# Kernel optimization log

Hardware: AMD Instinct MI355X
Metric: run time of the kernel (lower is better)

The kernel has to match this reference:

```python
import jax, jax.numpy as jnp
import numpy as np

N_NODES = 50000
N_EDGES = 800000
NODE_DIM = 128
EDGE_IN = 31
EMB_DIM = 128
GATE_HID = 128
INIT_GATE_BIAS = 2.0


def setup_inputs() -> dict:
    key = jax.random.key(0)
    ks = jax.random.split(key, 8)
    x = jax.random.normal(ks[0], (N_NODES, NODE_DIM), dtype=jnp.float32)
    edge_attr = jax.random.normal(ks[1], (N_EDGES, EDGE_IN), dtype=jnp.float32)
    edge_index = jax.random.randint(ks[2], (2, N_EDGES), 0, N_NODES, dtype=jnp.int64)
    gate_in_dim = 2 * NODE_DIM + EDGE_IN
    # params (torch.nn.Linear-style scaled uniform init)
    def lin(k, fan_in, fan_out):
        bound = 1.0 / np.sqrt(fan_in)
        kw, kb = jax.random.split(k)
        W = jax.random.uniform(kw, (fan_in, fan_out), minval=-bound, maxval=bound, dtype=jnp.float32)
        b = jax.random.uniform(kb, (fan_out,), minval=-bound, maxval=bound, dtype=jnp.float32)
        return W, b
    W_proj, b_proj = lin(ks[3], EDGE_IN, EMB_DIM)
    W1, b1 = lin(ks[4], gate_in_dim, GATE_HID)
    W2, _ = lin(ks[5], GATE_HID, 1)
    b2 = jnp.full((1,), INIT_GATE_BIAS, dtype=jnp.float32)
    return {
        "x": x,
        "edge_attr": edge_attr,
        "edge_index": edge_index,
        "W_proj": W_proj,
        "b_proj": b_proj,
        "W1": W1,
        "b1": b1,
        "W2": W2,
        "b2": b2,
    }


def reference(x, edge_attr, edge_index, W_proj, b_proj, W1, b1, W2, b2):
    src = edge_index[0]
    dst = edge_index[1]
    xu = x[src]                      # [E, node_dim] gather
    xv = x[dst]                      # [E, node_dim] gather
    base = edge_attr @ W_proj + b_proj            # [E, emb_dim]
    gate_in = jnp.concatenate([xu, xv, edge_attr], axis=-1)  # [E, 2*node_dim+31]
    h = jax.nn.gelu(gate_in @ W1 + b1)            # [E, gate_hidden]
    gate = jax.nn.sigmoid(h @ W2 + b2)            # [E, 1]
    return base * gate                            # [E, emb_dim]
```

## Files before the change

### kernel.cpp

```cpp
#include <hip/hip_runtime.h>
#include <math.h>

#define N_NODES 50000
#define N_EDGES 800000

typedef __attribute__((ext_vector_type(8))) short bf16x8;
typedef __attribute__((ext_vector_type(4))) float f32x4;

__device__ __forceinline__ unsigned f2bfu(float f) {
  union { float f; unsigned u; } v; v.f = f;
  return (v.u + 0x7FFFu + ((v.u >> 16) & 1u)) >> 16;
}
__device__ __forceinline__ short f2bf(float f) { return (short)f2bfu(f); }

__device__ __forceinline__ float bflo(unsigned d) {
  union { unsigned u; float f; } v; v.u = d << 16; return v.f;
}
__device__ __forceinline__ float bfhi(unsigned d) {
  union { unsigned u; float f; } v; v.u = d & 0xFFFF0000u; return v.f;
}

__device__ __forceinline__ float gelu_f(float h) {
  const float m1 = h * h;
  const float t2u = h * fmaf(0.07135481f, m1, 1.5957691f);
  const float e = __expf(t2u);
  const float rc = __builtin_amdgcn_rcpf(1.f + e);
  return h - h * rc;
}

#define PIN(v) asm volatile("" : "+v"(v))

__global__ void wfrag_kernel(const float* __restrict__ W_proj,
                             const float* __restrict__ W1,
                             uint4* __restrict__ wfrag) {
  const int id = threadIdx.x;
  const int mat = id >> 9;
  const int fid = id & 511;
  const int mb = fid >> 6, ln = fid & 63;
  const int rr = ln & 15, gg = ln >> 4;
  const float* W = mat ? W_proj : (W1 + (size_t)256 * 128);
  union { uint4 u; bf16x8 b; } f;
#pragma unroll
  for (int t = 0; t < 8; ++t) {
    const int kk = gg * 8 + t;
    f.b[t] = (kk < 31) ? f2bf(W[(size_t)kk * 128 + 16 * mb + rr]) : (short)0;
  }
  wfrag[id] = f.u;
}

__global__ __launch_bounds__(256) void node_kernel(
    const float* __restrict__ x, const float* __restrict__ W1,
    const float* __restrict__ b1, unsigned short* __restrict__ AB) {
  const int l = threadIdx.x & 63;
  const int wv = threadIdx.x >> 6;
  const int r = l & 15, g4 = l >> 4;

  const int wid = blockIdx.x * 4 + wv;
  const int s = wid & 3;

  bf16x8 wA[4][4];
#pragma unroll
  for (int q = 0; q < 4; ++q) {
    const int c = 16 * (4 * s + q) + r;
    const float* Wb = (c < 128) ? (W1 + c) : (W1 + 128 * 128 + (c - 128));
#pragma unroll
    for (int ks = 0; ks < 4; ++ks) {
#pragma unroll
      for (int t = 0; t < 8; ++t)
        wA[q][ks][t] = f2bf(Wb[(size_t)(ks * 32 + g4 * 8 + t) * 128]);
      PIN(wA[q][ks]);
    }
  }
  float4 bv[4];
#pragma unroll
  for (int q = 0; q < 4; ++q)
    bv[q] = *(const float4*)(b1 + ((16 * (4 * s + q) + g4 * 4) & 127));

  const int half = s >> 1;

  for (int t0 = wid >> 2; t0 < (N_NODES / 16); t0 += 1024) {
    const int n0 = t0 * 16;
    f32x4 acc[4] = {{0,0,0,0},{0,0,0,0},{0,0,0,0},{0,0,0,0}};
#pragma unroll
    for (int ks = 0; ks < 4; ++ks) {
      const float* xr = x + (size_t)(n0 + r) * 128 + ks * 32 + g4 * 8;
      const float4 x0 = *(const float4*)xr;
      const float4 x1 = *(const float4*)(xr + 4);
      bf16x8 xb;
      xb[0] = f2bf(x0.x); xb[1] = f2bf(x0.y); xb[2] = f2bf(x0.z); xb[3] = f2bf(x0.w);
      xb[4] = f2bf(x1.x); xb[5] = f2bf(x1.y); xb[6] = f2bf(x1.z); xb[7] = f2bf(x1.w);
#pragma unroll
      for (int q = 0; q < 4; ++q)
        acc[q] = __builtin_amdgcn_mfma_f32_16x16x32_bf16(wA[q][ks], xb, acc[q], 0, 0, 0);
    }
#pragma unroll
    for (int q = 0; q < 4; ++q) {
      const int mb8 = 4 * (s & 1) + q;
      const float o0 = acc[q][0] + 0.5f * bv[q].x;
      const float o1 = acc[q][1] + 0.5f * bv[q].y;
      const float o2 = acc[q][2] + 0.5f * bv[q].z;
      const float o3 = acc[q][3] + 0.5f * bv[q].w;
      uint2 pk;
      pk.x = f2bfu(o0) | (f2bfu(o1) << 16);
      pk.y = f2bfu(o2) | (f2bfu(o3) << 16);
      *(uint2*)(AB + (size_t)(n0 + r) * 256 + half * 128 + g4 * 32 + mb8 * 4) = pk;
    }
  }
}

__global__ __launch_bounds__(256) void edge_kernel(
    const float* __restrict__ edge_attr, const int* __restrict__ edge_index,
    const unsigned short* __restrict__ AB, const uint4* __restrict__ wfrag,
    const float* __restrict__ b_proj, const float* __restrict__ W2,
    const float* __restrict__ b2, float* __restrict__ out) {
  __shared__ float tlds[4][16 * 128];
  const int l = threadIdx.x & 63;
  const int wv = threadIdx.x >> 6;
  const int r = l & 15, g4 = l >> 4;
  float* const tl = &tlds[wv][0];

  bf16x8 wH[8];
#pragma unroll
  for (int mb = 0; mb < 8; ++mb) {
    union { uint4 u; bf16x8 b; } h;
    h.u = wfrag[mb * 64 + l];
    wH[mb] = h.b;
    PIN(wH[mb]);
  }
  const float b2v = b2[0];
  const uint4* wpp = wfrag + 512;

  const int nwaves = gridDim.x * 4;
  const int NT = N_EDGES / 16;

  int tile = blockIdx.x * 4 + wv;
  if (tile >= NT) return;
  int src = edge_index[tile * 16 + r];
  int dst = edge_index[N_EDGES + tile * 16 + r];

  for (; tile < NT; tile += nwaves) {
    const int e = tile * 16 + r;
    const int cs = src, cd = dst;

    const int tn = tile + nwaves;
    if (tn < NT) {
      src = edge_index[tn * 16 + r];
      dst = edge_index[N_EDGES + tn * 16 + r];
    }

    const float* ear = edge_attr + (size_t)e * 31 + g4 * 8;
    bf16x8 eb;
#pragma unroll
    for (int t = 0; t < 8; ++t) {
      const int kk = g4 * 8 + t;
      eb[t] = (kk < 31) ? f2bf(ear[t]) : (short)0;
    }

    const uint4* ap4 = (const uint4*)(AB + (size_t)cs * 256 + g4 * 32);
    const uint4* bp4 = (const uint4*)(AB + (size_t)cd * 256 + 128 + g4 * 32);
    uint4 ua[4], ub[4];
#pragma unroll
    for (int t = 0; t < 4; ++t) { ua[t] = ap4[t]; ub[t] = bp4[t]; }

    f32x4 acch[8];
#pragma unroll
    for (int t = 0; t < 4; ++t) {
      acch[2 * t][0]     = bflo(ua[t].x) + bflo(ub[t].x);
      acch[2 * t][1]     = bfhi(ua[t].x) + bfhi(ub[t].x);
      acch[2 * t][2]     = bflo(ua[t].y) + bflo(ub[t].y);
      acch[2 * t][3]     = bfhi(ua[t].y) + bfhi(ub[t].y);
      acch[2 * t + 1][0] = bflo(ua[t].z) + bflo(ub[t].z);
      acch[2 * t + 1][1] = bfhi(ua[t].z) + bfhi(ub[t].z);
      acch[2 * t + 1][2] = bflo(ua[t].w) + bflo(ub[t].w);
      acch[2 * t + 1][3] = bfhi(ua[t].w) + bfhi(ub[t].w);
    }
#pragma unroll
    for (int mb = 0; mb < 8; ++mb)
      acch[mb] = __builtin_amdgcn_mfma_f32_16x16x32_bf16(wH[mb], eb, acch[mb], 0, 0, 0);

    float lg = 0.f;
#pragma unroll
    for (int mb = 0; mb < 8; ++mb) {
      const float4 w2v = *(const float4*)(W2 + 16 * mb + g4 * 4);
      lg = fmaf(gelu_f(acch[mb][0]), w2v.x, lg);
      lg = fmaf(gelu_f(acch[mb][1]), w2v.y, lg);
      lg = fmaf(gelu_f(acch[mb][2]), w2v.z, lg);
      lg = fmaf(gelu_f(acch[mb][3]), w2v.w, lg);
    }
    lg += __shfl_xor(lg, 16);
    lg += __shfl_xor(lg, 32);
    const float gate = __builtin_amdgcn_rcpf(1.f + __expf(-(lg + b2v)));

    PIN(wpp);

#pragma unroll
    for (int mb = 0; mb < 8; ++mb) {
      union { uint4 u; bf16x8 b; } wp;
      wp.u = wpp[mb * 64 + l];
      f32x4 ac = __builtin_amdgcn_mfma_f32_16x16x32_bf16(
          wp.b, eb, (f32x4){0.f, 0.f, 0.f, 0.f}, 0, 0, 0);
      const float4 bp = *(const float4*)(b_proj + 16 * mb + 4 * g4);
      f32x4 o;
      o[0] = (ac[0] + bp.x) * gate;
      o[1] = (ac[1] + bp.y) * gate;
      o[2] = (ac[2] + bp.z) * gate;
      o[3] = (ac[3] + bp.w) * gate;
      const int col = 16 * mb + 4 * g4;
      *(f32x4*)(tl + 128 * r + (col ^ ((r & 7) << 2))) = o;
    }

    float* const obase = out + (size_t)tile * 16 * 128;
#pragma unroll
    for (int k = 0; k < 8; ++k) {
      const int row = 2 * k + (l >> 5);
      const int col = 4 * (l & 31);
      const f32x4 v = *(const f32x4*)(tl + 128 * row + (col ^ ((row & 7) << 2)));
      __builtin_nontemporal_store(v, (f32x4*)(obase + 256 * k + 4 * l));
    }
  }
}

extern "C" void kernel_launch(void* const* d_in, const int* in_sizes, int n_in,
                              void* d_out, int out_size, void* d_ws, size_t ws_size,
                              hipStream_t stream) {
  const float* x          = (const float*)d_in[0];
  const float* edge_attr  = (const float*)d_in[1];
  const int*   edge_index = (const int*)d_in[2];
  const float* W_proj     = (const float*)d_in[3];
  const float* b_proj     = (const float*)d_in[4];
  const float* W1         = (const float*)d_in[5];
  const float* b1         = (const float*)d_in[6];
  const float* W2         = (const float*)d_in[7];
  const float* b2         = (const float*)d_in[8];
  float* out = (float*)d_out;
  unsigned short* AB = (unsigned short*)d_ws;
  uint4* wfrag = (uint4*)(AB + (size_t)N_NODES * 256);

  hipLaunchKernelGGL(wfrag_kernel, dim3(1), dim3(1024), 0, stream,
                     W_proj, W1, wfrag);
  hipLaunchKernelGGL(node_kernel, dim3(1024), dim3(256), 0, stream,
                     x, W1, b1, AB);
  hipLaunchKernelGGL(edge_kernel, dim3(2048), dim3(256), 0, stream,
                     edge_attr, edge_index, AB, wfrag, b_proj, W2, b2,
                     out);
}
```

Before: 190.6 us.

## Software-pipeline edge gathers one tile ahead, fold b_proj into MFMA, stage W_proj in LDS

The edge kernel now prefetches the next tile's node-row gathers and edge attributes into registers while computing the current tile, with edge indices fetched two tiles ahead, so gather latency overlaps compute. The projection bias is folded into the W_proj fragment as a 32nd K-row multiplied by a constant 1.0 lane in the edge-attribute operand, removing the per-tile bias loads and adds. The W_proj fragments are staged once per block into shared memory instead of being reloaded from global memory each tile. This raises register pressure and LDS use, which may lower occupancy, and the bias is now rounded to bf16.

```diff
diff --git a/kernel.cpp b/kernel.cpp
--- a/kernel.cpp
+++ b/kernel.cpp
@@ -32,6 +32,7 @@
 
 __global__ void wfrag_kernel(const float* __restrict__ W_proj,
                              const float* __restrict__ W1,
+                             const float* __restrict__ b_proj,
                              uint4* __restrict__ wfrag) {
   const int id = threadIdx.x;
   const int mat = id >> 9;
@@ -43,7 +44,10 @@
 #pragma unroll
   for (int t = 0; t < 8; ++t) {
     const int kk = gg * 8 + t;
-    f.b[t] = (kk < 31) ? f2bf(W[(size_t)kk * 128 + 16 * mb + rr]) : (short)0;
+    float v = 0.f;
+    if (kk < 31) v = W[(size_t)kk * 128 + 16 * mb + rr];
+    else if (mat == 1 && kk == 31) v = b_proj[16 * mb + rr];
+    f.b[t] = f2bf(v);
   }
   wfrag[id] = f.u;
 }
@@ -111,13 +115,18 @@
 __global__ __launch_bounds__(256) void edge_kernel(
     const float* __restrict__ edge_attr, const int* __restrict__ edge_index,
     const unsigned short* __restrict__ AB, const uint4* __restrict__ wfrag,
-    const float* __restrict__ b_proj, const float* __restrict__ W2,
-    const float* __restrict__ b2, float* __restrict__ out) {
+    const float* __restrict__ W2, const float* __restrict__ b2,
+    float* __restrict__ out) {
   __shared__ float tlds[4][16 * 128];
-  const int l = threadIdx.x & 63;
-  const int wv = threadIdx.x >> 6;
+  __shared__ uint4 wPl[512];
+  const int tid = threadIdx.x;
+  const int l = tid & 63;
+  const int wv = tid >> 6;
   const int r = l & 15, g4 = l >> 4;
   float* const tl = &tlds[wv][0];
+
+  wPl[tid] = wfrag[512 + tid];
+  wPl[tid + 256] = wfrag[768 + tid];
 
   bf16x8 wH[8];
 #pragma unroll
@@ -128,39 +137,47 @@
     PIN(wH[mb]);
   }
   const float b2v = b2[0];
-  const uint4* wpp = wfrag + 512;
+  __syncthreads();
 
   const int nwaves = gridDim.x * 4;
   const int NT = N_EDGES / 16;
 
   int tile = blockIdx.x * 4 + wv;
   if (tile >= NT) return;
-  int src = edge_index[tile * 16 + r];
-  int dst = edge_index[N_EDGES + tile * 16 + r];
-
-  for (; tile < NT; tile += nwaves) {
+
+  int sA, dA;
+  uint4 ua[4], ub[4];
+  float ear[8];
+  {
     const int e = tile * 16 + r;
-    const int cs = src, cd = dst;
-
-    const int tn = tile + nwaves;
-    if (tn < NT) {
-      src = edge_index[tn * 16 + r];
-      dst = edge_index[N_EDGES + tn * 16 + r];
-    }
-
-    const float* ear = edge_attr + (size_t)e * 31 + g4 * 8;
-    bf16x8 eb;
-#pragma unroll
-    for (int t = 0; t < 8; ++t) {
-      const int kk = g4 * 8 + t;
-      eb[t] = (kk < 31) ? f2bf(ear[t]) : (short)0;
-    }
-
+    const int cs = edge_index[e];
+    const int cd = edge_index[N_EDGES + e];
     const uint4* ap4 = (const uint4*)(AB + (size_t)cs * 256 + g4 * 32);
     const uint4* bp4 = (const uint4*)(AB + (size_t)cd * 256 + 128 + g4 * 32);
-    uint4 ua[4], ub[4];
 #pragma unroll
     for (int t = 0; t < 4; ++t) { ua[t] = ap4[t]; ub[t] = bp4[t]; }
+    const float* earp = edge_attr + (size_t)e * 31 + g4 * 8;
+#pragma unroll
+    for (int t = 0; t < 8; ++t)
+      ear[t] = (g4 * 8 + t < 31) ? earp[t] : 0.f;
+    const int tn = tile + nwaves;
+    const int en = (tn < NT ? tn : tile) * 16 + r;
+    sA = edge_index[en];
+    dA = edge_index[N_EDGES + en];
+  }
+
+  for (; tile < NT; tile += nwaves) {
+    const int tn = tile + nwaves;
+    const int tn2 = tile + 2 * nwaves;
+
+    const int en2 = (tn2 < NT ? tn2 : tile) * 16 + r;
+    const int sB = edge_index[en2];
+    const int dB = edge_index[N_EDGES + en2];
+
+    bf16x8 eb;
+#pragma unroll
+    for (int t = 0; t < 8; ++t) eb[t] = f2bf(ear[t]);
+    if (g4 == 3) eb[7] = (short)0x3F80;
 
     f32x4 acch[8];
 #pragma unroll
@@ -174,6 +191,18 @@
       acch[2 * t + 1][2] = bflo(ua[t].w) + bflo(ub[t].w);
       acch[2 * t + 1][3] = bfhi(ua[t].w) + bfhi(ub[t].w);
     }
+
+    if (tn < NT) {
+      const uint4* ap4 = (const uint4*)(AB + (size_t)sA * 256 + g4 * 32);
+      const uint4* bp4 = (const uint4*)(AB + (size_t)dA * 256 + 128 + g4 * 32);
+#pragma unroll
+      for (int t = 0; t < 4; ++t) { ua[t] = ap4[t]; ub[t] = bp4[t]; }
+      const float* earp = edge_attr + (size_t)(tn * 16 + r) * 31 + g4 * 8;
+#pragma unroll
+      for (int t = 0; t < 8; ++t)
+        if (g4 * 8 + t < 31) ear[t] = earp[t];
+    }
+
 #pragma unroll
     for (int mb = 0; mb < 8; ++mb)
       acch[mb] = __builtin_amdgcn_mfma_f32_16x16x32_bf16(wH[mb], eb, acch[mb], 0, 0, 0);
@@ -181,7 +210,7 @@
     float lg = 0.f;
 #pragma unroll
     for (int mb = 0; mb < 8; ++mb) {
-      const float4 w2v = *(const float4*)(W2 + 16 * mb + g4 * 4);
+      const float4 w2v = *(const float4*)(W2 + 16 * mb + 4 * g4);
       lg = fmaf(gelu_f(acch[mb][0]), w2v.x, lg);
       lg = fmaf(gelu_f(acch[mb][1]), w2v.y, lg);
       lg = fmaf(gelu_f(acch[mb][2]), w2v.z, lg);
@@ -191,20 +220,20 @@
     lg += __shfl_xor(lg, 32);
     const float gate = __builtin_amdgcn_rcpf(1.f + __expf(-(lg + b2v)));
 
-    PIN(wpp);
+    unsigned zoff = 0;
+    PIN(zoff);
 
 #pragma unroll
     for (int mb = 0; mb < 8; ++mb) {
       union { uint4 u; bf16x8 b; } wp;
-      wp.u = wpp[mb * 64 + l];
+      wp.u = wPl[mb * 64 + l + zoff];
       f32x4 ac = __builtin_amdgcn_mfma_f32_16x16x32_bf16(
           wp.b, eb, (f32x4){0.f, 0.f, 0.f, 0.f}, 0, 0, 0);
-      const float4 bp = *(const float4*)(b_proj + 16 * mb + 4 * g4);
       f32x4 o;
-      o[0] = (ac[0] + bp.x) * gate;
-      o[1] = (ac[1] + bp.y) * gate;
-      o[2] = (ac[2] + bp.z) * gate;
-      o[3] = (ac[3] + bp.w) * gate;
+      o[0] = ac[0] * gate;
+      o[1] = ac[1] * gate;
+      o[2] = ac[2] * gate;
+      o[3] = ac[3] * gate;
       const int col = 16 * mb + 4 * g4;
       *(f32x4*)(tl + 128 * r + (col ^ ((r & 7) << 2))) = o;
     }
@@ -217,6 +246,8 @@
       const f32x4 v = *(const f32x4*)(tl + 128 * row + (col ^ ((row & 7) << 2)));
       __builtin_nontemporal_store(v, (f32x4*)(obase + 256 * k + 4 * l));
     }
+
+    sA = sB; dA = dB;
   }
 }
 
@@ -237,10 +268,10 @@
   uint4* wfrag = (uint4*)(AB + (size_t)N_NODES * 256);
 
   hipLaunchKernelGGL(wfrag_kernel, dim3(1), dim3(1024), 0, stream,
-                     W_proj, W1, wfrag);
+                     W_proj, W1, b_proj, wfrag);
   hipLaunchKernelGGL(node_kernel, dim3(1024), dim3(256), 0, stream,
                      x, W1, b1, AB);
   hipLaunchKernelGGL(edge_kernel, dim3(2048), dim3(256), 0, stream,
-                     edge_attr, edge_index, AB, wfrag, b_proj, W2, b2,
+                     edge_attr, edge_index, AB, wfrag, W2, b2,
                      out);
 }
```

After: 171.4 us. 10.1% less time.
